# Optimization experiments

Measured on AMD Instinct MI355X. Metric: run time of the kernel, lower is better.

The kernel has to match this reference:

```python
import jax, jax.numpy as jnp
import numpy as np

N_NODES = 100000
N_EDGES = 3200000
C_IN = 128
C_OUT = 128
K = 4

def setup_inputs() -> dict:
    key = jax.random.key(0)
    k1, k2, k3, k4, k5 = jax.random.split(key, 5)
    x = jax.random.normal(k1, (N_NODES, C_IN), dtype=jnp.float32)
    # per-edge Laplacian values, scaled so the Chebyshev recurrence stays bounded
    lap = jax.random.normal(k2, (N_EDGES,), dtype=jnp.float32) * 0.05
    stdv = 1.0 / np.sqrt(C_IN * K)
    weight = jax.random.uniform(k3, (K, C_IN, C_OUT), dtype=jnp.float32, minval=-stdv, maxval=stdv)
    bias = jax.random.uniform(k4, (C_OUT,), dtype=jnp.float32, minval=-stdv, maxval=stdv)
    edge_index = jax.random.randint(k5, (2, N_EDGES), 0, N_NODES, dtype=jnp.int64)
    return {"x": x, "lap": lap, "weight": weight, "bias": bias,
            "edge_index": edge_index, "num_nodes": N_NODES}

def _spmm(edge_index, lap, num_nodes, x):
    # y[row] += lap_e * x[col] for each edge e = (row, col)
    row, col = edge_index[0], edge_index[1]
    msgs = lap[:, None] * x[col]            # [E, C]
    return jax.ops.segment_sum(msgs, row, num_segments=num_nodes)

def reference(x, lap, weight, bias, edge_index, num_nodes):
    K_ = weight.shape[0]
    Tx_0 = x                                 # T_0(L) x = x
    out = Tx_0 @ weight[0]
    if K_ > 1:
        Tx_1 = _spmm(edge_index, lap, num_nodes, x)   # T_1(L) x = L x
        out = out + Tx_1 @ weight[1]
    for k in range(2, K_):
        Tx_2 = 2.0 * _spmm(edge_index, lap, num_nodes, Tx_1) - Tx_0
        out = out + Tx_2 @ weight[k]
        Tx_0, Tx_1 = Tx_1, Tx_2
    return out + bias
```

## Files before the change

### kernel.cpp

```cpp
#include <hip/hip_runtime.h>

#define N_NODES 100000
#define N_EDGES 3200000
#define ROWS_PAD 100032
#define N_BUCKETS 782
#define BUCKET_SHIFT 7

typedef __attribute__((ext_vector_type(8))) short bf16x8;
typedef __attribute__((ext_vector_type(4))) float f32x4;
typedef __attribute__((ext_vector_type(2))) float f32x2;

__device__ __forceinline__ unsigned short f2bf(float f) {
    unsigned u = __float_as_uint(f);
    unsigned r = (u + 0x7fffu + ((u >> 16) & 1u)) >> 16;
    return (unsigned short)r;
}
__device__ __forceinline__ float bflo(unsigned u) { return __uint_as_float(u << 16); }
__device__ __forceinline__ float bfhi(unsigned u) { return __uint_as_float(u & 0xffff0000u); }

__global__ void __launch_bounds__(256) k_convert_x(const float* __restrict__ x,
                                                   unsigned* __restrict__ xf8) {
    const int QTOT = ROWS_PAD * 32;
    for (int q = blockIdx.x * 256 + threadIdx.x; q < QTOT; q += 1024 * 256) {
        int r = q >> 5;
        f32x4 f = {0.f, 0.f, 0.f, 0.f};
        if (r < N_NODES) f = *(const f32x4*)(x + 4 * (size_t)q);
        int pk = __builtin_amdgcn_cvt_pk_fp8_f32(f.x, f.y, 0, false);
        pk = __builtin_amdgcn_cvt_pk_fp8_f32(f.z, f.w, pk, true);
        xf8[q] = (unsigned)pk;
    }
}

__global__ void k_convert_w(const float* __restrict__ w, unsigned short* __restrict__ wt) {
    int i = blockIdx.x * 256 + threadIdx.x;
    int m = i >> 14, rem = i & 16383, k = rem >> 7, c = rem & 127;
    wt[(m << 14) + (c << 7) + k] = f2bf(w[i]);
}

__global__ void __launch_bounds__(256) k_bhist(const int* __restrict__ ei, int* __restrict__ bcnt) {
    __shared__ int h[N_BUCKETS];
    for (int i = threadIdx.x; i < N_BUCKETS; i += 256) h[i] = 0;
    __syncthreads();
    int base = blockIdx.x * 8192;
#pragma unroll
    for (int i = 0; i < 32; ++i) {
        int e = base + threadIdx.x + i * 256;
        if (e < N_EDGES) atomicAdd(&h[ei[e] >> BUCKET_SHIFT], 1);
    }
    __syncthreads();
    for (int i = threadIdx.x; i < N_BUCKETS; i += 256)
        if (h[i]) atomicAdd(&bcnt[i], h[i]);
}

__global__ void __launch_bounds__(1024) k_bscan(const int* __restrict__ bcnt,
                                                int* __restrict__ bbase,
                                                int* __restrict__ bcursor,
                                                int* __restrict__ rowstart,
                                                int2* __restrict__ ep) {
    __shared__ int s[1024];
    int t = threadIdx.x;
    int v = (t < N_BUCKETS) ? bcnt[t] : 0;
    s[t] = v;
    __syncthreads();
    for (int off = 1; off < 1024; off <<= 1) {
        int tv = (t >= off) ? s[t - off] : 0;
        __syncthreads();
        s[t] += tv;
        __syncthreads();
    }
    if (t < N_BUCKETS) {
        int ex = s[t] - v;
        bbase[t] = ex;
        bcursor[t] = ex;
    }
    if (t == 0) {
        bbase[N_BUCKETS] = N_EDGES;
        rowstart[N_NODES] = N_EDGES;
    }
    if (t < 64) ep[N_EDGES + t] = make_int2(0, 0);
}

__global__ void __launch_bounds__(1024) k_bin(const int* __restrict__ ei,
                                              const float* __restrict__ lap,
                                              int* __restrict__ bcursor,
                                              uint2* __restrict__ ep_tmp) {
    __shared__ int h[N_BUCKETS];
    __shared__ int runbase[N_BUCKETS];
    for (int i = threadIdx.x; i < N_BUCKETS; i += 1024) h[i] = 0;
    __syncthreads();
    int base = blockIdx.x * 16384;
#pragma unroll
    for (int i = 0; i < 16; ++i) {
        int e = base + threadIdx.x + i * 1024;
        if (e < N_EDGES) atomicAdd(&h[ei[e] >> BUCKET_SHIFT], 1);
    }
    __syncthreads();
    for (int i = threadIdx.x; i < N_BUCKETS; i += 1024) {
        int c = h[i];
        runbase[i] = c ? atomicAdd(&bcursor[i], c) : 0;
        h[i] = 0;
    }
    __syncthreads();
#pragma unroll
    for (int i = 0; i < 16; ++i) {
        int e = base + threadIdx.x + i * 1024;
        if (e < N_EDGES) {
            int row = ei[e], col = ei[N_EDGES + e];
            int b = row >> BUCKET_SHIFT;
            int p = runbase[b] + atomicAdd(&h[b], 1);
            ep_tmp[p] = make_uint2(((unsigned)(row & 127) << 17) | (unsigned)col,
                                   __float_as_uint(lap[e]));
        }
    }
}

#define ST_CAP 5120
__global__ void __launch_bounds__(256) k_rsort(const uint2* __restrict__ ep_tmp,
                                               const int* __restrict__ bbase,
                                               int* __restrict__ rowstart,
                                               int2* __restrict__ ep) {
    __shared__ uint2 st[ST_CAP];
    __shared__ int h[128];
    __shared__ int lcur[128];
    int b = blockIdx.x;
    int base = bbase[b], end = bbase[b + 1];
    int n = end - base;
    if (n > ST_CAP) n = ST_CAP;
    for (int i = threadIdx.x; i < n; i += 256) st[i] = ep_tmp[base + i];
    if (threadIdx.x < 128) h[threadIdx.x] = 0;
    __syncthreads();
    for (int i = threadIdx.x; i < n; i += 256) atomicAdd(&h[st[i].x >> 17], 1);
    __syncthreads();
    int t = threadIdx.x;
    int v = (t < 128) ? h[t] : 0;
    for (int off = 1; off < 128; off <<= 1) {
        int tv = (t < 128 && t >= off) ? h[t - off] : 0;
        __syncthreads();
        if (t < 128) h[t] += tv;
        __syncthreads();
    }
    if (t < 128) {
        int ex = h[t] - v;
        int r = (b << BUCKET_SHIFT) + t;
        if (r < N_NODES) rowstart[r] = base + ex;
        lcur[t] = base + ex;
    }
    __syncthreads();
    for (int i = threadIdx.x; i < n; i += 256) {
        uint2 s = st[i];
        int r = s.x >> 17;
        int p = atomicAdd(&lcur[r], 1);
        ep[p] = make_int2((int)(s.x & 0x1FFFFu), (int)s.y);
    }
}

__global__ void __launch_bounds__(256) k_spmm8(
    const unsigned char* __restrict__ xs, const void* __restrict__ z, int zmode,
    unsigned* __restrict__ y8, uint2* __restrict__ yb,
    const int* __restrict__ rowstart, const int2* __restrict__ ep, float a, float b)
{
    int wv = threadIdx.x >> 6, lane = threadIdx.x & 63;
    int r = blockIdx.x * 4 + wv;
    if (r >= N_NODES) return;
    int q = lane >> 4, s = lane & 15;
    unsigned vs8 = (unsigned)s * 8u;
    int bp0 = (q) * 4, bp1 = (4 + q) * 4, bp2 = (8 + q) * 4, bp3 = (12 + q) * 4;
    float acc0 = 0.f, acc1 = 0.f, acc2 = 0.f, acc3 = 0.f;
    float acc4 = 0.f, acc5 = 0.f, acc6 = 0.f, acc7 = 0.f;
    int e0 = rowstart[r], e1 = rowstart[r + 1];
    int cnt = e1 - e0;
    if (cnt > 0) {
        int niter = (cnt + 15) >> 4;
        int nfull = cnt >> 4;
        const char* epb = (const char*)ep;

#define LOADEP(p, itv) do {                                              \
        int _idx = e0 + (itv) * 16 + s;                                  \
        int2 _t = *(const int2*)(epb + (unsigned)_idx * 8u);             \
        if ((itv) >= nfull) {                   \
            bool _v = _idx < e1;                                         \
            _t.x = _v ? _t.x : 0;          \
            _t.y = _v ? _t.y : 0;         \
        }                                                                \
        p = _t;                                                          \
    } while (0)
#define BPERM(cc, ll, p) do {                                            \
        cc[0] = __builtin_amdgcn_ds_bpermute(bp0, (p).x);                \
        cc[1] = __builtin_amdgcn_ds_bpermute(bp1, (p).x);                \
        cc[2] = __builtin_amdgcn_ds_bpermute(bp2, (p).x);                \
        cc[3] = __builtin_amdgcn_ds_bpermute(bp3, (p).x);                \
        ll[0] = __builtin_amdgcn_ds_bpermute(bp0, (p).y);                \
        ll[1] = __builtin_amdgcn_ds_bpermute(bp1, (p).y);                \
        ll[2] = __builtin_amdgcn_ds_bpermute(bp2, (p).y);                \
        ll[3] = __builtin_amdgcn_ds_bpermute(bp3, (p).y);                \
    } while (0)
#define GATHER(G, cc) do {                                               \
        _Pragma("unroll")                                                \
        for (int _u = 0; _u < 4; ++_u)                                   \
            G[_u] = *(const uint2*)(xs + ((((unsigned)cc[_u]) << 7) + vs8)); \
    } while (0)
#define CONSUME(G, ll) do {                                              \
        _Pragma("unroll")                                                \
        for (int _u = 0; _u < 4; ++_u) {                                 \
            float _l = __int_as_float(ll[_u]);                           \
            f32x2 _f0 = __builtin_amdgcn_cvt_pk_f32_fp8((int)G[_u].x, false); \
            f32x2 _f1 = __builtin_amdgcn_cvt_pk_f32_fp8((int)G[_u].x, true);  \
            f32x2 _f2 = __builtin_amdgcn_cvt_pk_f32_fp8((int)G[_u].y, false); \
            f32x2 _f3 = __builtin_amdgcn_cvt_pk_f32_fp8((int)G[_u].y, true);  \
            acc0 += _l * _f0.x; acc1 += _l * _f0.y;                      \
            acc2 += _l * _f1.x; acc3 += _l * _f1.y;                      \
            acc4 += _l * _f2.x; acc5 += _l * _f2.y;                      \
            acc6 += _l * _f3.x; acc7 += _l * _f3.y;                      \
        }                                                                \
    } while (0)

        int2 pA, pB;
        int cA[4], cB[4], lA[4], lB[4];
        uint2 GA[4], GB[4];

        LOADEP(pA, 0);
        BPERM(cA, lA, pA);
        GATHER(GA, cA);
        int it = 0;
        while (it + 2 <= niter) {
            LOADEP(pB, it + 1);
            BPERM(cB, lB, pB);
            GATHER(GB, cB);
            CONSUME(GA, lA);
            if (it + 2 < niter) {
                LOADEP(pA, it + 2);
                BPERM(cA, lA, pA);
                GATHER(GA, cA);
            }
            CONSUME(GB, lB);
            it += 2;
        }
        if (it < niter) CONSUME(GA, lA);
#undef LOADEP
#undef BPERM
#undef GATHER
#undef CONSUME
    }
    acc0 += __shfl(acc0, lane ^ 16, 64); acc1 += __shfl(acc1, lane ^ 16, 64);
    acc2 += __shfl(acc2, lane ^ 16, 64); acc3 += __shfl(acc3, lane ^ 16, 64);
    acc4 += __shfl(acc4, lane ^ 16, 64); acc5 += __shfl(acc5, lane ^ 16, 64);
    acc6 += __shfl(acc6, lane ^ 16, 64); acc7 += __shfl(acc7, lane ^ 16, 64);
    acc0 += __shfl(acc0, lane ^ 32, 64); acc1 += __shfl(acc1, lane ^ 32, 64);
    acc2 += __shfl(acc2, lane ^ 32, 64); acc3 += __shfl(acc3, lane ^ 32, 64);
    acc4 += __shfl(acc4, lane ^ 32, 64); acc5 += __shfl(acc5, lane ^ 32, 64);
    acc6 += __shfl(acc6, lane ^ 32, 64); acc7 += __shfl(acc7, lane ^ 32, 64);
    if (q == 0) {
        float o0 = a * acc0, o1 = a * acc1, o2 = a * acc2, o3 = a * acc3;
        float o4 = a * acc4, o5 = a * acc5, o6 = a * acc6, o7 = a * acc7;
        if (zmode == 1) {
            uint4 zg = *((const uint4*)z + (size_t)r * 16 + s);
            o0 += b * bflo(zg.x); o1 += b * bfhi(zg.x);
            o2 += b * bflo(zg.y); o3 += b * bfhi(zg.y);
            o4 += b * bflo(zg.z); o5 += b * bfhi(zg.z);
            o6 += b * bflo(zg.w); o7 += b * bfhi(zg.w);
        } else if (zmode == 3) {
            const f32x4* zp = (const f32x4*)z + (size_t)r * 32 + s * 2;
            f32x4 z0 = zp[0], z1 = zp[1];
            o0 += b * z0.x; o1 += b * z0.y; o2 += b * z0.z; o3 += b * z0.w;
            o4 += b * z1.x; o5 += b * z1.y; o6 += b * z1.z; o7 += b * z1.w;
        }
        uint4 ob;
        ob.x = (unsigned)f2bf(o0) | ((unsigned)f2bf(o1) << 16);
        ob.y = (unsigned)f2bf(o2) | ((unsigned)f2bf(o3) << 16);
        ob.z = (unsigned)f2bf(o4) | ((unsigned)f2bf(o5) << 16);
        ob.w = (unsigned)f2bf(o6) | ((unsigned)f2bf(o7) << 16);
        *((uint4*)yb + (size_t)r * 16 + s) = ob;
        if (y8) {
            int pk0 = __builtin_amdgcn_cvt_pk_fp8_f32(o0, o1, 0, false);
            pk0 = __builtin_amdgcn_cvt_pk_fp8_f32(o2, o3, pk0, true);
            int pk1 = __builtin_amdgcn_cvt_pk_fp8_f32(o4, o5, 0, false);
            pk1 = __builtin_amdgcn_cvt_pk_fp8_f32(o6, o7, pk1, true);
            *((uint2*)y8 + (size_t)r * 16 + s) = make_uint2((unsigned)pk0, (unsigned)pk1);
        }
    }
}

__global__ void __launch_bounds__(256, 2) k_gemm4(
    const float* __restrict__ x,
    const unsigned short* __restrict__ t1,
    const unsigned short* __restrict__ t2,
    const unsigned short* __restrict__ t3,
    const unsigned short* __restrict__ wt,
    float* __restrict__ out, const float* __restrict__ bias)
{
    __shared__ uint4 ldsq[4096];
    char* lds = (char*)ldsq;
    int wv = threadIdx.x >> 6, lane = threadIdx.x & 63;
    int m = lane & 15, quad = lane >> 4;
    int r0 = blockIdx.x * 64 + wv * 16;
    int row = r0 + m;
    int rowc = (row >= N_NODES) ? (N_NODES - 1) : row;

    bf16x8 a0[4], a1[4], a2[4], a3[4];
    {
        const float* p = x + (size_t)rowc * 128 + quad * 8;
#pragma unroll
        for (int kk = 0; kk < 4; ++kk) {
            f32x4 u = *(const f32x4*)(p + kk * 32);
            f32x4 v = *(const f32x4*)(p + kk * 32 + 4);
            bf16x8 fr;
            fr[0] = (short)f2bf(u.x); fr[1] = (short)f2bf(u.y);
            fr[2] = (short)f2bf(u.z); fr[3] = (short)f2bf(u.w);
            fr[4] = (short)f2bf(v.x); fr[5] = (short)f2bf(v.y);
            fr[6] = (short)f2bf(v.z); fr[7] = (short)f2bf(v.w);
            a0[kk] = fr;
        }
    }
    {
        const short* p = (const short*)t1 + (size_t)row * 128 + quad * 8;
#pragma unroll
        for (int kk = 0; kk < 4; ++kk) a1[kk] = *(const bf16x8*)(p + kk * 32);
    }
    {
        const short* p = (const short*)t2 + (size_t)row * 128 + quad * 8;
#pragma unroll
        for (int kk = 0; kk < 4; ++kk) a2[kk] = *(const bf16x8*)(p + kk * 32);
    }
    {
        const short* p = (const short*)t3 + (size_t)row * 128 + quad * 8;
#pragma unroll
        for (int kk = 0; kk < 4; ++kk) a3[kk] = *(const bf16x8*)(p + kk * 32);
    }

    f32x4 acc[8];
#pragma unroll
    for (int ct = 0; ct < 8; ++ct) acc[ct] = (f32x4){0.f, 0.f, 0.f, 0.f};

#pragma unroll
    for (int ph = 0; ph < 2; ++ph) {
        if (ph) __syncthreads();
        const char* src = (const char*)wt + ph * 65536;
#pragma unroll
        for (int i = 0; i < 16; ++i) {
            int idx = i * 256 + (int)threadIdx.x;
            int g = idx >> 4, j = idx & 15;
            *(uint4*)(lds + g * 256 + ((unsigned)(j ^ (g & 15)) << 4)) =
                *(const uint4*)(src + idx * 16);
        }
        __syncthreads();
#pragma unroll
        for (int tl = 0; tl < 2; ++tl) {
#pragma unroll
            for (int ct = 0; ct < 8; ++ct) {
#pragma unroll
                for (int kk = 0; kk < 4; ++kk) {
                    const bf16x8* B = (const bf16x8*)(lds + tl * 32768 + ct * 4096
                        + m * 256 + ((unsigned)(((quad + kk * 4) ^ m)) << 4));
                    bf16x8 av = (ph == 0) ? (tl == 0 ? a0[kk] : a1[kk])
                                          : (tl == 0 ? a2[kk] : a3[kk]);
                    acc[ct] = __builtin_amdgcn_mfma_f32_16x16x32_bf16(av, *B, acc[ct], 0, 0, 0);
                }
            }
        }
    }
    __syncthreads();
    float* cw = (float*)lds + wv * (16 * 132);
#pragma unroll
    for (int ct = 0; ct < 8; ++ct)
#pragma unroll
        for (int i = 0; i < 4; ++i)
            cw[(quad * 4 + i) * 132 + ct * 16 + m] = acc[ct][i];
    int er = lane >> 2, ec = (lane & 3) * 32;
    int gr = r0 + er;
#pragma unroll
    for (int j = 0; j < 8; ++j) {
        f32x4 v = *(f32x4*)(cw + er * 132 + ec + j * 4);
        f32x4 bb = *(const f32x4*)(bias + ec + j * 4);
        v.x += bb.x; v.y += bb.y; v.z += bb.z; v.w += bb.w;
        if (gr < N_NODES)
            *(f32x4*)(out + (size_t)gr * 128 + ec + j * 4) = v;
    }
}

extern "C" void kernel_launch(void* const* d_in, const int* in_sizes, int n_in,
                              void* d_out, int out_size, void* d_ws, size_t ws_size,
                              hipStream_t stream) {
    const float* x    = (const float*)d_in[0];
    const float* lap  = (const float*)d_in[1];
    const float* w    = (const float*)d_in[2];
    const float* bias = (const float*)d_in[3];
    const int*   ei   = (const int*)d_in[4];
    float* out = (float*)d_out;

    char* ws = (char*)d_ws;
    const size_t SZ_BF = (size_t)ROWS_PAD * 128 * 2;
    const size_t SZ_F8 = (size_t)ROWS_PAD * 128;
    const size_t SZ_EP = SZ_BF + 1024;
    int2* ep            = (int2*)(ws);
    unsigned char* xf8  = (unsigned char*)(ws + SZ_EP);
    unsigned char* t1_8 = (unsigned char*)(ws + SZ_EP + SZ_F8);
    unsigned char* t3_b = (unsigned char*)(ws + SZ_EP);
    unsigned char* t1_b = (unsigned char*)(ws + SZ_EP + SZ_BF);
    unsigned char* t2_8 = (unsigned char*)(ws + SZ_EP + 2 * SZ_BF);
    unsigned char* t2_b = (unsigned char*)(ws + SZ_EP + 2 * SZ_BF + SZ_F8);
    uint2* ep_tmp       = (uint2*)(ws + SZ_EP + 2 * SZ_BF);
    char* p = ws + SZ_EP + 3 * SZ_BF + SZ_F8;
    int* rowstart = (int*)p; p += 400128;
    int* bcnt     = (int*)p; p += 3200;
    int* bbase    = (int*)p; p += 3200;
    int* bcursor  = (int*)p; p += 3200;
    unsigned short* wt = (unsigned short*)p;

    hipMemsetAsync(bcnt, 0, N_BUCKETS * sizeof(int), stream);
    k_convert_x<<<1024, 256, 0, stream>>>(x, (unsigned*)xf8);
    k_convert_w<<<256, 256, 0, stream>>>(w, wt);
    k_bhist<<<(N_EDGES + 8191) / 8192, 256, 0, stream>>>(ei, bcnt);
    k_bscan<<<1, 1024, 0, stream>>>(bcnt, bbase, bcursor, rowstart, ep);
    k_bin<<<(N_EDGES + 16383) / 16384, 1024, 0, stream>>>(ei, lap, bcursor, ep_tmp);
    k_rsort<<<N_BUCKETS, 256, 0, stream>>>(ep_tmp, bbase, rowstart, ep);

    k_spmm8<<<ROWS_PAD / 4, 256, 0, stream>>>(xf8, nullptr, 0,
        (unsigned*)t1_8, (uint2*)t1_b, rowstart, ep, 1.f, 0.f);
    k_spmm8<<<ROWS_PAD / 4, 256, 0, stream>>>(t1_8, x, 3,
        (unsigned*)t2_8, (uint2*)t2_b, rowstart, ep, 2.f, -1.f);
    k_spmm8<<<ROWS_PAD / 4, 256, 0, stream>>>(t2_8, t1_b, 1,
        nullptr, (uint2*)t3_b, rowstart, ep, 2.f, -1.f);
    k_gemm4<<<ROWS_PAD / 64, 256, 0, stream>>>(x, (const unsigned short*)t1_b,
        (const unsigned short*)t2_b, (const unsigned short*)t3_b, wt, out, bias);
}
```

Measured before the change: 502.0 us.

## Process two rows per wavefront in SpMM and halve edge-binning block size

The SpMM kernel now has each wavefront handle two adjacent rows at once, interleaving their edge loads, permutes and gathers. This doubles the memory requests in flight per wave and hides gather latency on the average-degree-32 rows. The padding zeroed past the edge array grows from 64 to 1024 entries so reads beyond the end stay safe. Separately, the binning kernel uses 8192 edges per block instead of 16384, which doubles the grid. The costs are higher register pressure and lost work when the two rows have different lengths.

```diff
diff --git a/kernel.cpp b/kernel.cpp
--- a/kernel.cpp
+++ b/kernel.cpp
@@ -77,7 +77,7 @@
         bbase[N_BUCKETS] = N_EDGES;
         rowstart[N_NODES] = N_EDGES;
     }
-    if (t < 64) ep[N_EDGES + t] = make_int2(0, 0);
+    ep[N_EDGES + t] = make_int2(0, 0);
 }
 
 __global__ void __launch_bounds__(1024) k_bin(const int* __restrict__ ei,
@@ -88,9 +88,9 @@
     __shared__ int runbase[N_BUCKETS];
     for (int i = threadIdx.x; i < N_BUCKETS; i += 1024) h[i] = 0;
     __syncthreads();
-    int base = blockIdx.x * 16384;
-#pragma unroll
-    for (int i = 0; i < 16; ++i) {
+    int base = blockIdx.x * 8192;
+#pragma unroll
+    for (int i = 0; i < 8; ++i) {
         int e = base + threadIdx.x + i * 1024;
         if (e < N_EDGES) atomicAdd(&h[ei[e] >> BUCKET_SHIFT], 1);
     }
@@ -102,7 +102,7 @@
     }
     __syncthreads();
 #pragma unroll
-    for (int i = 0; i < 16; ++i) {
+    for (int i = 0; i < 8; ++i) {
         int e = base + threadIdx.x + i * 1024;
         if (e < N_EDGES) {
             int row = ei[e], col = ei[N_EDGES + e];
@@ -160,122 +160,148 @@
     const int* __restrict__ rowstart, const int2* __restrict__ ep, float a, float b)
 {
     int wv = threadIdx.x >> 6, lane = threadIdx.x & 63;
-    int r = blockIdx.x * 4 + wv;
-    if (r >= N_NODES) return;
+    int r0 = blockIdx.x * 8 + wv * 2;
+    if (r0 >= N_NODES) return;
     int q = lane >> 4, s = lane & 15;
     unsigned vs8 = (unsigned)s * 8u;
     int bp0 = (q) * 4, bp1 = (4 + q) * 4, bp2 = (8 + q) * 4, bp3 = (12 + q) * 4;
-    float acc0 = 0.f, acc1 = 0.f, acc2 = 0.f, acc3 = 0.f;
-    float acc4 = 0.f, acc5 = 0.f, acc6 = 0.f, acc7 = 0.f;
-    int e0 = rowstart[r], e1 = rowstart[r + 1];
-    int cnt = e1 - e0;
-    if (cnt > 0) {
-        int niter = (cnt + 15) >> 4;
-        int nfull = cnt >> 4;
-        const char* epb = (const char*)ep;
-
-#define LOADEP(p, itv) do {                                              \
-        int _idx = e0 + (itv) * 16 + s;                                  \
-        int2 _t = *(const int2*)(epb + (unsigned)_idx * 8u);             \
-        if ((itv) >= nfull) {                   \
-            bool _v = _idx < e1;                                         \
-            _t.x = _v ? _t.x : 0;          \
-            _t.y = _v ? _t.y : 0;         \
-        }                                                                \
-        p = _t;                                                          \
-    } while (0)
-#define BPERM(cc, ll, p) do {                                            \
-        cc[0] = __builtin_amdgcn_ds_bpermute(bp0, (p).x);                \
-        cc[1] = __builtin_amdgcn_ds_bpermute(bp1, (p).x);                \
-        cc[2] = __builtin_amdgcn_ds_bpermute(bp2, (p).x);                \
-        cc[3] = __builtin_amdgcn_ds_bpermute(bp3, (p).x);                \
-        ll[0] = __builtin_amdgcn_ds_bpermute(bp0, (p).y);                \
-        ll[1] = __builtin_amdgcn_ds_bpermute(bp1, (p).y);                \
-        ll[2] = __builtin_amdgcn_ds_bpermute(bp2, (p).y);                \
-        ll[3] = __builtin_amdgcn_ds_bpermute(bp3, (p).y);                \
-    } while (0)
-#define GATHER(G, cc) do {                                               \
+    const char* epb = (const char*)ep;
+
+    int e0[2], e1[2], nfull[2];
+    e0[0] = rowstart[r0]; e1[0] = rowstart[r0 + 1];
+    bool has1 = (r0 + 1) < N_NODES;
+    e0[1] = has1 ? e1[0] : N_EDGES;
+    e1[1] = has1 ? rowstart[r0 + 2] : N_EDGES;
+    int niter = 0;
+#pragma unroll
+    for (int c = 0; c < 2; ++c) {
+        int cnt = e1[c] - e0[c];
+        nfull[c] = cnt > 0 ? (cnt >> 4) : 0;
+        int ni = cnt > 0 ? ((cnt + 15) >> 4) : 0;
+        if (ni > niter) niter = ni;
+    }
+    float acc[2][8];
+#pragma unroll
+    for (int c = 0; c < 2; ++c)
+#pragma unroll
+        for (int k = 0; k < 8; ++k) acc[c][k] = 0.f;
+
+    if (niter > 0) {
+#define LOADEP(P, itv) do {                                              \
         _Pragma("unroll")                                                \
-        for (int _u = 0; _u < 4; ++_u)                                   \
-            G[_u] = *(const uint2*)(xs + ((((unsigned)cc[_u]) << 7) + vs8)); \
-    } while (0)
-#define CONSUME(G, ll) do {                                              \
+        for (int _c = 0; _c < 2; ++_c) {                                 \
+            int _idx = e0[_c] + (itv) * 16 + s;                          \
+            int2 _t = *(const int2*)(epb + (unsigned)_idx * 8u);         \
+            if ((itv) >= nfull[_c]) {           \
+                bool _v = _idx < e1[_c];                                 \
+                _t.x = _v ? _t.x : 0;      \
+                _t.y = _v ? _t.y : 0;     \
+            }                                                            \
+            P[_c] = _t;                                                  \
+        } } while (0)
+#define BPERM(C, L, P) do {                                              \
         _Pragma("unroll")                                                \
-        for (int _u = 0; _u < 4; ++_u) {                                 \
-            float _l = __int_as_float(ll[_u]);                           \
-            f32x2 _f0 = __builtin_amdgcn_cvt_pk_f32_fp8((int)G[_u].x, false); \
-            f32x2 _f1 = __builtin_amdgcn_cvt_pk_f32_fp8((int)G[_u].x, true);  \
-            f32x2 _f2 = __builtin_amdgcn_cvt_pk_f32_fp8((int)G[_u].y, false); \
-            f32x2 _f3 = __builtin_amdgcn_cvt_pk_f32_fp8((int)G[_u].y, true);  \
-            acc0 += _l * _f0.x; acc1 += _l * _f0.y;                      \
-            acc2 += _l * _f1.x; acc3 += _l * _f1.y;                      \
-            acc4 += _l * _f2.x; acc5 += _l * _f2.y;                      \
-            acc6 += _l * _f3.x; acc7 += _l * _f3.y;                      \
-        }                                                                \
-    } while (0)
-
-        int2 pA, pB;
-        int cA[4], cB[4], lA[4], lB[4];
-        uint2 GA[4], GB[4];
-
-        LOADEP(pA, 0);
-        BPERM(cA, lA, pA);
-        GATHER(GA, cA);
+        for (int _c = 0; _c < 2; ++_c) {                                 \
+            C[_c][0] = __builtin_amdgcn_ds_bpermute(bp0, P[_c].x);       \
+            C[_c][1] = __builtin_amdgcn_ds_bpermute(bp1, P[_c].x);       \
+            C[_c][2] = __builtin_amdgcn_ds_bpermute(bp2, P[_c].x);       \
+            C[_c][3] = __builtin_amdgcn_ds_bpermute(bp3, P[_c].x);       \
+            L[_c][0] = __builtin_amdgcn_ds_bpermute(bp0, P[_c].y);       \
+            L[_c][1] = __builtin_amdgcn_ds_bpermute(bp1, P[_c].y);       \
+            L[_c][2] = __builtin_amdgcn_ds_bpermute(bp2, P[_c].y);       \
+            L[_c][3] = __builtin_amdgcn_ds_bpermute(bp3, P[_c].y);       \
+        } } while (0)
+#define GATHER(G, C) do {                                                \
+        _Pragma("unroll")                                                \
+        for (int _c = 0; _c < 2; ++_c)                                   \
+            _Pragma("unroll")                                            \
+            for (int _u = 0; _u < 4; ++_u)                               \
+                G[_c][_u] = *(const uint2*)(xs + ((((unsigned)C[_c][_u]) << 7) + vs8)); \
+        } while (0)
+#define CONSUME(G, L) do {                                               \
+        _Pragma("unroll")                                                \
+        for (int _c = 0; _c < 2; ++_c)                                   \
+            _Pragma("unroll")                                            \
+            for (int _u = 0; _u < 4; ++_u) {                             \
+                float _l = __int_as_float(L[_c][_u]);                    \
+                f32x2 _f0 = __builtin_amdgcn_cvt_pk_f32_fp8((int)G[_c][_u].x, false); \
+                f32x2 _f1 = __builtin_amdgcn_cvt_pk_f32_fp8((int)G[_c][_u].x, true);  \
+                f32x2 _f2 = __builtin_amdgcn_cvt_pk_f32_fp8((int)G[_c][_u].y, false); \
+                f32x2 _f3 = __builtin_amdgcn_cvt_pk_f32_fp8((int)G[_c][_u].y, true);  \
+                acc[_c][0] += _l * _f0.x; acc[_c][1] += _l * _f0.y;      \
+                acc[_c][2] += _l * _f1.x; acc[_c][3] += _l * _f1.y;      \
+                acc[_c][4] += _l * _f2.x; acc[_c][5] += _l * _f2.y;      \
+                acc[_c][6] += _l * _f3.x; acc[_c][7] += _l * _f3.y;      \
+            }                                                            \
+        } while (0)
+
+        int2 PA[2], PB[2];
+        int CA[2][4], CB[2][4], LA[2][4], LB[2][4];
+        uint2 GA[2][4], GB[2][4];
+
+        LOADEP(PA, 0);
+        BPERM(CA, LA, PA);
+        GATHER(GA, CA);
         int it = 0;
         while (it + 2 <= niter) {
-            LOADEP(pB, it + 1);
-            BPERM(cB, lB, pB);
-            GATHER(GB, cB);
-            CONSUME(GA, lA);
+            LOADEP(PB, it + 1);
+            BPERM(CB, LB, PB);
+            GATHER(GB, CB);
+            CONSUME(GA, LA);
             if (it + 2 < niter) {
-                LOADEP(pA, it + 2);
-                BPERM(cA, lA, pA);
-                GATHER(GA, cA);
+                LOADEP(PA, it + 2);
+                BPERM(CA, LA, PA);
+                GATHER(GA, CA);
             }
-            CONSUME(GB, lB);
+            CONSUME(GB, LB);
             it += 2;
         }
-        if (it < niter) CONSUME(GA, lA);
+        if (it < niter) CONSUME(GA, LA);
 #undef LOADEP
 #undef BPERM
 #undef GATHER
 #undef CONSUME
     }
-    acc0 += __shfl(acc0, lane ^ 16, 64); acc1 += __shfl(acc1, lane ^ 16, 64);
-    acc2 += __shfl(acc2, lane ^ 16, 64); acc3 += __shfl(acc3, lane ^ 16, 64);
-    acc4 += __shfl(acc4, lane ^ 16, 64); acc5 += __shfl(acc5, lane ^ 16, 64);
-    acc6 += __shfl(acc6, lane ^ 16, 64); acc7 += __shfl(acc7, lane ^ 16, 64);
-    acc0 += __shfl(acc0, lane ^ 32, 64); acc1 += __shfl(acc1, lane ^ 32, 64);
-    acc2 += __shfl(acc2, lane ^ 32, 64); acc3 += __shfl(acc3, lane ^ 32, 64);
-    acc4 += __shfl(acc4, lane ^ 32, 64); acc5 += __shfl(acc5, lane ^ 32, 64);
-    acc6 += __shfl(acc6, lane ^ 32, 64); acc7 += __shfl(acc7, lane ^ 32, 64);
+#pragma unroll
+    for (int c = 0; c < 2; ++c) {
+#pragma unroll
+        for (int k = 0; k < 8; ++k) {
+            acc[c][k] += __shfl(acc[c][k], lane ^ 16, 64);
+            acc[c][k] += __shfl(acc[c][k], lane ^ 32, 64);
+        }
+    }
     if (q == 0) {
-        float o0 = a * acc0, o1 = a * acc1, o2 = a * acc2, o3 = a * acc3;
-        float o4 = a * acc4, o5 = a * acc5, o6 = a * acc6, o7 = a * acc7;
-        if (zmode == 1) {
-            uint4 zg = *((const uint4*)z + (size_t)r * 16 + s);
-            o0 += b * bflo(zg.x); o1 += b * bfhi(zg.x);
-            o2 += b * bflo(zg.y); o3 += b * bfhi(zg.y);
-            o4 += b * bflo(zg.z); o5 += b * bfhi(zg.z);
-            o6 += b * bflo(zg.w); o7 += b * bfhi(zg.w);
-        } else if (zmode == 3) {
-            const f32x4* zp = (const f32x4*)z + (size_t)r * 32 + s * 2;
-            f32x4 z0 = zp[0], z1 = zp[1];
-            o0 += b * z0.x; o1 += b * z0.y; o2 += b * z0.z; o3 += b * z0.w;
-            o4 += b * z1.x; o5 += b * z1.y; o6 += b * z1.z; o7 += b * z1.w;
-        }
-        uint4 ob;
-        ob.x = (unsigned)f2bf(o0) | ((unsigned)f2bf(o1) << 16);
-        ob.y = (unsigned)f2bf(o2) | ((unsigned)f2bf(o3) << 16);
-        ob.z = (unsigned)f2bf(o4) | ((unsigned)f2bf(o5) << 16);
-        ob.w = (unsigned)f2bf(o6) | ((unsigned)f2bf(o7) << 16);
-        *((uint4*)yb + (size_t)r * 16 + s) = ob;
-        if (y8) {
-            int pk0 = __builtin_amdgcn_cvt_pk_fp8_f32(o0, o1, 0, false);
-            pk0 = __builtin_amdgcn_cvt_pk_fp8_f32(o2, o3, pk0, true);
-            int pk1 = __builtin_amdgcn_cvt_pk_fp8_f32(o4, o5, 0, false);
-            pk1 = __builtin_amdgcn_cvt_pk_fp8_f32(o6, o7, pk1, true);
-            *((uint2*)y8 + (size_t)r * 16 + s) = make_uint2((unsigned)pk0, (unsigned)pk1);
+#pragma unroll
+        for (int c = 0; c < 2; ++c) {
+            int r = r0 + c;
+            if (r >= N_NODES) continue;
+            float o0 = a * acc[c][0], o1 = a * acc[c][1], o2 = a * acc[c][2], o3 = a * acc[c][3];
+            float o4 = a * acc[c][4], o5 = a * acc[c][5], o6 = a * acc[c][6], o7 = a * acc[c][7];
+            if (zmode == 1) {
+                uint4 zg = *((const uint4*)z + (size_t)r * 16 + s);
+                o0 += b * bflo(zg.x); o1 += b * bfhi(zg.x);
+                o2 += b * bflo(zg.y); o3 += b * bfhi(zg.y);
+                o4 += b * bflo(zg.z); o5 += b * bfhi(zg.z);
+                o6 += b * bflo(zg.w); o7 += b * bfhi(zg.w);
+            } else if (zmode == 3) {
+                const f32x4* zp = (const f32x4*)z + (size_t)r * 32 + s * 2;
+                f32x4 z0 = zp[0], z1 = zp[1];
+                o0 += b * z0.x; o1 += b * z0.y; o2 += b * z0.z; o3 += b * z0.w;
+                o4 += b * z1.x; o5 += b * z1.y; o6 += b * z1.z; o7 += b * z1.w;
+            }
+            uint4 ob;
+            ob.x = (unsigned)f2bf(o0) | ((unsigned)f2bf(o1) << 16);
+            ob.y = (unsigned)f2bf(o2) | ((unsigned)f2bf(o3) << 16);
+            ob.z = (unsigned)f2bf(o4) | ((unsigned)f2bf(o5) << 16);
+            ob.w = (unsigned)f2bf(o6) | ((unsigned)f2bf(o7) << 16);
+            *((uint4*)yb + (size_t)r * 16 + s) = ob;
+            if (y8) {
+                int pk0 = __builtin_amdgcn_cvt_pk_fp8_f32(o0, o1, 0, false);
+                pk0 = __builtin_amdgcn_cvt_pk_fp8_f32(o2, o3, pk0, true);
+                int pk1 = __builtin_amdgcn_cvt_pk_fp8_f32(o4, o5, 0, false);
+                pk1 = __builtin_amdgcn_cvt_pk_fp8_f32(o6, o7, pk1, true);
+                *((uint2*)y8 + (size_t)r * 16 + s) = make_uint2((unsigned)pk0, (unsigned)pk1);
+            }
         }
     }
 }
@@ -390,7 +416,7 @@
     char* ws = (char*)d_ws;
     const size_t SZ_BF = (size_t)ROWS_PAD * 128 * 2;
     const size_t SZ_F8 = (size_t)ROWS_PAD * 128;
-    const size_t SZ_EP = SZ_BF + 1024;
+    const size_t SZ_EP = SZ_BF + 8192;
     int2* ep            = (int2*)(ws);
     unsigned char* xf8  = (unsigned char*)(ws + SZ_EP);
     unsigned char* t1_8 = (unsigned char*)(ws + SZ_EP + SZ_F8);
@@ -411,14 +437,14 @@
     k_convert_w<<<256, 256, 0, stream>>>(w, wt);
     k_bhist<<<(N_EDGES + 8191) / 8192, 256, 0, stream>>>(ei, bcnt);
     k_bscan<<<1, 1024, 0, stream>>>(bcnt, bbase, bcursor, rowstart, ep);
-    k_bin<<<(N_EDGES + 16383) / 16384, 1024, 0, stream>>>(ei, lap, bcursor, ep_tmp);
+    k_bin<<<(N_EDGES + 8191) / 8192, 1024, 0, stream>>>(ei, lap, bcursor, ep_tmp);
     k_rsort<<<N_BUCKETS, 256, 0, stream>>>(ep_tmp, bbase, rowstart, ep);
 
-    k_spmm8<<<ROWS_PAD / 4, 256, 0, stream>>>(xf8, nullptr, 0,
+    k_spmm8<<<ROWS_PAD / 8, 256, 0, stream>>>(xf8, nullptr, 0,
         (unsigned*)t1_8, (uint2*)t1_b, rowstart, ep, 1.f, 0.f);
-    k_spmm8<<<ROWS_PAD / 4, 256, 0, stream>>>(t1_8, x, 3,
+    k_spmm8<<<ROWS_PAD / 8, 256, 0, stream>>>(t1_8, x, 3,
         (unsigned*)t2_8, (uint2*)t2_b, rowstart, ep, 2.f, -1.f);
-    k_spmm8<<<ROWS_PAD / 4, 256, 0, stream>>>(t2_8, t1_b, 1,
+    k_spmm8<<<ROWS_PAD / 8, 256, 0, stream>>>(t2_8, t1_b, 1,
         nullptr, (uint2*)t3_b, rowstart, ep, 2.f, -1.f);
     k_gemm4<<<ROWS_PAD / 64, 256, 0, stream>>>(x, (const unsigned short*)t1_b,
         (const unsigned short*)t2_b, (const unsigned short*)t3_b, wt, out, bias);
```

Result: slower. 514.8 us (+2.6%).
